# Optimization experiments

Hardware: AMD Instinct MI355X
Metric: run time of the kernel (lower is better)

Reference implementation:

```python
import jax, jax.numpy as jnp
import numpy as np

B, S, D, H = 8, 4096, 1024, 1024


def log_g(x):
    # log of g(x) = where(x>=0, x+0.5, sigmoid(x)); strictly positive
    return jnp.where(x >= 0, jnp.log(jax.nn.relu(x) + 0.5), -jax.nn.softplus(-x))


def mingru_layer(inp, W, b):
    # inp: (B,S,Din), W: (2H,Din), b: (2H,)
    gh = jnp.einsum('bsd,ed->bse', inp, W) + b
    gate, hidden = jnp.split(gh, 2, axis=2)          # each (B,S,H)
    log_z = -jax.nn.softplus(-gate)                   # log sigmoid(gate)
    log_coeffs = -jax.nn.softplus(gate)               # log(1 - sigmoid(gate))
    h0_log = jnp.full((inp.shape[0], 1, gate.shape[2]), jnp.log(0.5), inp.dtype)  # g(0)=0.5
    log_values = jnp.concatenate([h0_log, log_z + log_g(hidden)], axis=1)  # (B,S+1,H)
    # parallel scan in log space
    a_star = jnp.pad(jnp.cumsum(log_coeffs, axis=1), ((0, 0), (1, 0), (0, 0)))  # (B,S+1,H)
    log_h = a_star + jax.lax.cumlogsumexp(log_values - a_star, axis=1)
    return jnp.exp(log_h)[:, 1:]                      # (B,S,H)


def setup_inputs() -> dict:
    key = jax.random.key(0)
    k = jax.random.split(key, 5)
    s = 1.0 / np.sqrt(D)
    return {
        'x': jax.random.normal(k[0], (B, S, D), jnp.float32),
        'W0': jax.random.uniform(k[1], (2 * H, D), jnp.float32, -s, s),
        'b0': jax.random.uniform(k[2], (2 * H,), jnp.float32, -s, s),
        'W1': jax.random.uniform(k[3], (2 * H, H), jnp.float32, -s, s),
        'b1': jax.random.uniform(k[4], (2 * H,), jnp.float32, -s, s),
    }


def reference(x, W0, b0, W1, b1):
    h1 = mingru_layer(x, W0, b0)    # layer 0
    out = mingru_layer(h1, W1, b1)  # layer 1 (last)
    return out                      # (B,S,H)
```

## Files before the change

kernel.cpp:

```cpp
#include <hip/hip_runtime.h>
#include <hip/hip_bf16.h>
#include <stdint.h>


typedef __attribute__((ext_vector_type(8))) short bf16x8;
typedef __attribute__((ext_vector_type(4))) float f32x4;

__device__ __forceinline__ unsigned short f2bf(float f) {
    union { float f; unsigned int u; } x; x.f = f;
    unsigned int r = x.u + 0x7fffu + ((x.u >> 16) & 1u);
    return (unsigned short)(r >> 16);
}
__device__ __forceinline__ float bf2f(unsigned short u) {
    union { unsigned int i; float f; } x; x.i = ((unsigned int)u) << 16;
    return x.f;
}
__device__ __forceinline__ float fsig(float x) {
    return __builtin_amdgcn_rcpf(1.0f + __expf(-x));
}

__device__ __forceinline__ void async_cp16(const void* g, void* lds) {
    __builtin_amdgcn_global_load_lds(
        (const __attribute__((address_space(1))) unsigned int*)g,
        (__attribute__((address_space(3))) unsigned int*)lds, 16, 0, 0);
}

__global__ void f32_to_bf16_k(const float* __restrict__ in,
                              unsigned short* __restrict__ out, int n8) {
    int i = blockIdx.x * blockDim.x + threadIdx.x;
    if (i >= n8) return;
    const float4* p = reinterpret_cast<const float4*>(in);
    float4 a = p[2 * i], b = p[2 * i + 1];
    float f[8] = {a.x, a.y, a.z, a.w, b.x, b.y, b.z, b.w};
    union { unsigned short s[8]; uint4 v; } u;
#pragma unroll
    for (int j = 0; j < 8; ++j) u.s[j] = f2bf(f[j]);
    *reinterpret_cast<uint4*>(out + (size_t)i * 8) = u.v;
}

__global__ __launch_bounds__(512, 2) void gemm256(
    const short* __restrict__ A, const short* __restrict__ Wt,
    const float* __restrict__ bias, unsigned short* __restrict__ C,
    int M, int N, int K)
{
    __shared__ __align__(16) short lds_a[32768];
    __shared__ __align__(16) short lds_b[32768];

    const int tid  = threadIdx.x;
    const int lane = tid & 63;
    const int wave = tid >> 6;
    const int wm   = wave >> 2;
    const int wn   = wave & 3;

    const int bid  = blockIdx.x;
    const int slot = bid >> 3;
    const int mt   = (bid & 7) * 16 + (slot >> 3);
    const int nt   = slot & 7;
    const int m0   = mt * 256, n0 = nt * 256;

    const int g    = lane >> 4;
    const int x7   = lane & 7;
    const int r15  = lane & 15;
    const int aoff0 = (wm*128 + r15)*64 + (( g      ^ x7) * 8);
    const int aoff1 = (wm*128 + r15)*64 + (((4 + g) ^ x7) * 8);
    const int boff0 = (wn*64  + r15)*64 + (( g      ^ x7) * 8);
    const int boff1 = (wn*64  + r15)*64 + (((4 + g) ^ x7) * 8);

    const int srow = wave*16 + (lane >> 3);
    const int lch  = (lane & 7) ^ (lane >> 3);
    const short* pAs = A  + (size_t)(m0 + srow) * K + lch*8;
    const short* pBs = Wt + (size_t)(n0 + srow) * K + lch*8;
    const int dst = wave * 1024;

    f32x4  acc[8][4] = {};
    bf16x8 Ar[4][2];
    bf16x8 Br[2][2][2];

#define STG_A(h, kt) do { \
    async_cp16(pAs + (size_t)((h)*128    )*K + (kt)*64, lds_a + ((((kt)&1)*16384) + (h)*8192 + dst      )); \
    async_cp16(pAs + (size_t)((h)*128 + 8)*K + (kt)*64, lds_a + ((((kt)&1)*16384) + (h)*8192 + dst + 512)); } while (0)
#define STG_B(h, kt) do { \
    async_cp16(pBs + (size_t)((h)*128    )*K + (kt)*64, lds_b + ((((kt)&1)*16384) + (h)*8192 + dst      )); \
    async_cp16(pBs + (size_t)((h)*128 + 8)*K + (kt)*64, lds_b + ((((kt)&1)*16384) + (h)*8192 + dst + 512)); } while (0)

#define READ_A(mh, buf) do { _Pragma("unroll") \
    for (int f = 0; f < 4; ++f) { \
        Ar[f][0] = *reinterpret_cast<const bf16x8*>(lds_a + (buf)*16384 + (mh)*4096 + f*1024 + aoff0); \
        Ar[f][1] = *reinterpret_cast<const bf16x8*>(lds_a + (buf)*16384 + (mh)*4096 + f*1024 + aoff1); } } while (0)
#define READ_B(nh, buf) do { _Pragma("unroll") \
    for (int n = 0; n < 2; ++n) { \
        Br[nh][n][0] = *reinterpret_cast<const bf16x8*>(lds_b + (buf)*16384 + (nh)*2048 + n*1024 + boff0); \
        Br[nh][n][1] = *reinterpret_cast<const bf16x8*>(lds_b + (buf)*16384 + (nh)*2048 + n*1024 + boff1); } } while (0)

#define MFMA_Q(mh, nh) do { \
    __builtin_amdgcn_s_setprio(1); \
    _Pragma("unroll") for (int f = 0; f < 4; ++f) \
    _Pragma("unroll") for (int n = 0; n < 2; ++n) { \
        acc[(mh)*4+f][(nh)*2+n] = __builtin_amdgcn_mfma_f32_16x16x32_bf16(Ar[f][0], Br[nh][n][0], acc[(mh)*4+f][(nh)*2+n], 0, 0, 0); \
        acc[(mh)*4+f][(nh)*2+n] = __builtin_amdgcn_mfma_f32_16x16x32_bf16(Ar[f][1], Br[nh][n][1], acc[(mh)*4+f][(nh)*2+n], 0, 0, 0); } \
    __builtin_amdgcn_s_setprio(0); } while (0)

#define SB() __builtin_amdgcn_sched_barrier(0)
#define BAR1() do { SB(); __builtin_amdgcn_s_barrier(); \
    asm volatile("s_waitcnt lgkmcnt(0)" ::: "memory"); SB(); } while (0)
#define BAR2() do { SB(); __builtin_amdgcn_s_barrier(); \
    asm volatile("" ::: "memory"); SB(); } while (0)
#define VMW(n) asm volatile("s_waitcnt vmcnt(" #n ")" ::: "memory")

    STG_B(0, 0); STG_B(1, 0); STG_A(0, 0); STG_A(1, 0);
    STG_B(0, 1); STG_B(1, 1);
    VMW(4);
    BAR2();

#pragma unroll 1
    for (int i = 0; i < 7; ++i) {
        const int kt = 2 * i;
        READ_A(0,0); READ_B(0,0); STG_A(0, kt+1); BAR1(); MFMA_Q(0,0);         BAR2();
        READ_B(1,0);              STG_A(1, kt+1); BAR1(); MFMA_Q(0,1);         BAR2();
        READ_A(1,0);              STG_B(0, kt+2); BAR1(); MFMA_Q(1,0);         BAR2();
                                  STG_B(1, kt+2); BAR1(); MFMA_Q(1,1); VMW(4); BAR2();
        READ_A(0,1); READ_B(0,1); STG_A(0, kt+2); BAR1(); MFMA_Q(0,0);         BAR2();
        READ_B(1,1);              STG_A(1, kt+2); BAR1(); MFMA_Q(0,1);         BAR2();
        READ_A(1,1);              STG_B(0, kt+3); BAR1(); MFMA_Q(1,0);         BAR2();
                                  STG_B(1, kt+3); BAR1(); MFMA_Q(1,1); VMW(4); BAR2();
    }
    READ_A(0,0); READ_B(0,0); STG_A(0, 15); BAR1(); MFMA_Q(0,0);         BAR2();
    READ_B(1,0);              STG_A(1, 15); BAR1(); MFMA_Q(0,1);         BAR2();
    READ_A(1,0);                            BAR1(); MFMA_Q(1,0);         BAR2();
                                            BAR1(); MFMA_Q(1,1); VMW(0); BAR2();
    READ_A(0,1); READ_B(0,1);               BAR1(); MFMA_Q(0,0);         BAR2();
    READ_B(1,1);                            BAR1(); MFMA_Q(0,1);         BAR2();
    READ_A(1,1);                            BAR1(); MFMA_Q(1,0);         BAR2();
                                            BAR1(); MFMA_Q(1,1);        BAR2();

    const int quad  = lane >> 4;
    const int ccol0 = n0 + wn*64 + r15;
    const size_t crow0 = (size_t)(m0 + wm*128 + quad*4);
    float bv[4];
#pragma unroll
    for (int n = 0; n < 4; ++n) bv[n] = bias[ccol0 + n*16];
#pragma unroll
    for (int f = 0; f < 8; ++f)
#pragma unroll
        for (int r = 0; r < 4; ++r) {
            const size_t row = crow0 + f*16 + r;
#pragma unroll
            for (int n = 0; n < 4; ++n)
                C[row * N + ccol0 + n*16] = f2bf(acc[f][n][r] + bv[n]);
        }
#undef STG_A
#undef STG_B
#undef READ_A
#undef READ_B
#undef MFMA_Q
#undef SB
#undef BAR1
#undef BAR2
#undef VMW
}

__global__ void scan_partial(const unsigned short* __restrict__ gh,
                             float* __restrict__ P, float* __restrict__ V) {
    const int h4 = threadIdx.x;
    const int j = blockIdx.y, b = blockIdx.z;
    const size_t base = ((size_t)b * 4096 + (size_t)j * 32) * 2048 + h4 * 4;
    float p[4] = {1, 1, 1, 1}, hl[4] = {0, 0, 0, 0};
#pragma unroll 8
    for (int t = 0; t < 32; ++t) {
        ushort4 g  = *reinterpret_cast<const ushort4*>(gh + base + (size_t)t * 2048);
        ushort4 hd = *reinterpret_cast<const ushort4*>(gh + base + (size_t)t * 2048 + 1024);
        const unsigned short ga[4] = {g.x, g.y, g.z, g.w};
        const unsigned short ha[4] = {hd.x, hd.y, hd.z, hd.w};
#pragma unroll
        for (int c = 0; c < 4; ++c) {
            float gf = bf2f(ga[c]), hf = bf2f(ha[c]);
            float z  = fsig(gf);
            float cc = 1.0f - z;
            float gv = (hf >= 0.0f) ? (hf + 0.5f) : fsig(hf);
            p[c]  = p[c] * cc;
            hl[c] = cc * hl[c] + z * gv;
        }
    }
    const int ch = b * 1024 + h4 * 4;
    *reinterpret_cast<float4*>(P + (size_t)j * 8192 + ch) = make_float4(p[0], p[1], p[2], p[3]);
    *reinterpret_cast<float4*>(V + (size_t)j * 8192 + ch) = make_float4(hl[0], hl[1], hl[2], hl[3]);
}

__global__ void scan_combine(const float* __restrict__ P,
                             const float* __restrict__ V,
                             float* __restrict__ hstart) {
    const int c4 = blockIdx.x * blockDim.x + threadIdx.x;
    float4 h = make_float4(0.5f, 0.5f, 0.5f, 0.5f);
#pragma unroll 8
    for (int j = 0; j < 128; ++j) {
        *reinterpret_cast<float4*>(hstart + (size_t)j * 8192 + c4 * 4) = h;
        float4 pp = *reinterpret_cast<const float4*>(P + (size_t)j * 8192 + c4 * 4);
        float4 vv = *reinterpret_cast<const float4*>(V + (size_t)j * 8192 + c4 * 4);
        h.x = pp.x * h.x + vv.x; h.y = pp.y * h.y + vv.y;
        h.z = pp.z * h.z + vv.z; h.w = pp.w * h.w + vv.w;
    }
}

template <bool BF16OUT, typename OUT>
__global__ void scan_final(const unsigned short* __restrict__ gh,
                           const float* __restrict__ hstart,
                           OUT* __restrict__ out) {
    const int h4 = threadIdx.x;
    const int j = blockIdx.y, b = blockIdx.z;
    const size_t base  = ((size_t)b * 4096 + (size_t)j * 32) * 2048 + h4 * 4;
    const size_t obase = ((size_t)b * 4096 + (size_t)j * 32) * 1024 + h4 * 4;
    float4 hq = *reinterpret_cast<const float4*>(hstart + (size_t)j * 8192 + b * 1024 + h4 * 4);
    float hv[4] = {hq.x, hq.y, hq.z, hq.w};
#pragma unroll 8
    for (int t = 0; t < 32; ++t) {
        ushort4 g  = *reinterpret_cast<const ushort4*>(gh + base + (size_t)t * 2048);
        ushort4 hd = *reinterpret_cast<const ushort4*>(gh + base + (size_t)t * 2048 + 1024);
        const unsigned short ga[4] = {g.x, g.y, g.z, g.w};
        const unsigned short ha[4] = {hd.x, hd.y, hd.z, hd.w};
#pragma unroll
        for (int c = 0; c < 4; ++c) {
            float gf = bf2f(ga[c]), hf = bf2f(ha[c]);
            float z  = fsig(gf);
            float cc = 1.0f - z;
            float gv = (hf >= 0.0f) ? (hf + 0.5f) : fsig(hf);
            hv[c] = cc * hv[c] + z * gv;
        }
        if (BF16OUT) {
            ushort4 o = make_ushort4(f2bf(hv[0]), f2bf(hv[1]), f2bf(hv[2]), f2bf(hv[3]));
            *reinterpret_cast<ushort4*>((unsigned short*)out + obase + (size_t)t * 1024) = o;
        } else {
            *reinterpret_cast<float4*>((float*)out + obase + (size_t)t * 1024) =
                make_float4(hv[0], hv[1], hv[2], hv[3]);
        }
    }
}

extern "C" void kernel_launch(void* const* d_in, const int* in_sizes, int n_in,
                              void* d_out, int out_size, void* d_ws, size_t ws_size,
                              hipStream_t stream) {
    const float* x  = (const float*)d_in[0];
    const float* W0 = (const float*)d_in[1];
    const float* b0 = (const float*)d_in[2];
    const float* W1 = (const float*)d_in[3];
    const float* b1 = (const float*)d_in[4];
    float* out = (float*)d_out;

    char* ws = (char*)d_ws;
    unsigned short* gh   = (unsigned short*)ws;
    unsigned short* abuf = (unsigned short*)(ws + 0x08000000);
    unsigned short* w0b  = (unsigned short*)(ws + 0x0C000000);
    unsigned short* w1b  = (unsigned short*)(ws + 0x0C400000);
    float*          P    = (float*)(ws + 0x0C800000);
    float*          V    = (float*)(ws + 0x0CC00000);
    float*          hst  = (float*)(ws + 0x0D000000);

    const int M = 32768, N = 2048, K = 1024;

    f32_to_bf16_k<<<4194304 / 256, 256, 0, stream>>>(x,  abuf, 4194304);
    f32_to_bf16_k<<<262144 / 256, 256, 0, stream>>>(W0, w0b, 262144);
    f32_to_bf16_k<<<262144 / 256, 256, 0, stream>>>(W1, w1b, 262144);

    dim3 sg(1, 128, 8);

    gemm256<<<1024, 512, 0, stream>>>((const short*)abuf, (const short*)w0b, b0, gh, M, N, K);
    scan_partial<<<sg, 256, 0, stream>>>(gh, P, V);
    scan_combine<<<8, 256, 0, stream>>>(P, V, hst);
    scan_final<true, unsigned short><<<sg, 256, 0, stream>>>(gh, hst, abuf);

    gemm256<<<1024, 512, 0, stream>>>((const short*)abuf, (const short*)w1b, b1, gh, M, N, K);
    scan_partial<<<sg, 256, 0, stream>>>(gh, P, V);
    scan_combine<<<8, 256, 0, stream>>>(P, V, hst);
    scan_final<false, float><<<sg, 256, 0, stream>>>(gh, hst, out);
}
```

Measured before the change: 666.9 us.

## Restructure GEMM main loop barriers and widen scan combine parallelism

The GEMM inner loop is rebuilt from eight double-barrier phases per k-step pair into single-barrier phases. Global-to-LDS staging of A is moved to a per-block end point with a vmcnt wait, and the staging order and prologue depth change. The goal is to cut barrier count and give loads more room to overlap with MFMA work, at the risk of LDS hazards if buffer reuse timing is now wrong. Separately, scan_combine is split from float4-per-thread over 8 blocks into scalar-per-thread over 32 blocks, trading vector loads for more parallelism in its serial chain.

```diff
diff --git a/kernel.cpp b/kernel.cpp
--- a/kernel.cpp
+++ b/kernel.cpp
@@ -101,37 +101,50 @@
     __builtin_amdgcn_s_setprio(0); } while (0)
 
 #define SB() __builtin_amdgcn_sched_barrier(0)
-#define BAR1() do { SB(); __builtin_amdgcn_s_barrier(); \
-    asm volatile("s_waitcnt lgkmcnt(0)" ::: "memory"); SB(); } while (0)
-#define BAR2() do { SB(); __builtin_amdgcn_s_barrier(); \
-    asm volatile("" ::: "memory"); SB(); } while (0)
-#define VMW(n) asm volatile("s_waitcnt vmcnt(" #n ")" ::: "memory")
-
-    STG_B(0, 0); STG_B(1, 0); STG_A(0, 0); STG_A(1, 0);
-    STG_B(0, 1); STG_B(1, 1);
-    VMW(4);
-    BAR2();
+#define NOP ((void)0)
+#define PH0(b, STG) do { STG; READ_A(0,b); READ_B(0,b); SB(); \
+    __builtin_amdgcn_s_barrier(); \
+    asm volatile("s_waitcnt lgkmcnt(0)" ::: "memory"); SB(); MFMA_Q(0,0); } while (0)
+#define PH1(b) do { READ_B(1,b); SB(); \
+    __builtin_amdgcn_s_barrier(); \
+    asm volatile("s_waitcnt lgkmcnt(0)" ::: "memory"); SB(); MFMA_Q(0,1); } while (0)
+#define PH2(b) do { READ_A(1,b); SB(); \
+    __builtin_amdgcn_s_barrier(); \
+    asm volatile("s_waitcnt lgkmcnt(0)" ::: "memory"); SB(); MFMA_Q(1,0); } while (0)
+#define PH3(b, STG) do { STG; SB(); \
+    __builtin_amdgcn_s_barrier(); \
+    asm volatile("s_waitcnt lgkmcnt(0)" ::: "memory"); SB(); MFMA_Q(1,1); } while (0)
+#define ENDBLK(n, S1, S2) do { S1; S2; SB(); \
+    asm volatile("s_waitcnt vmcnt(" #n ")" ::: "memory"); \
+    __builtin_amdgcn_s_barrier(); SB(); } while (0)
+
+    STG_A(0, 0); STG_A(1, 0); STG_B(0, 0); STG_B(1, 0);
+    STG_B(0, 1); STG_A(0, 1); STG_A(1, 1);
+    ENDBLK(6, NOP, NOP);
 
 #pragma unroll 1
     for (int i = 0; i < 7; ++i) {
         const int kt = 2 * i;
-        READ_A(0,0); READ_B(0,0); STG_A(0, kt+1); BAR1(); MFMA_Q(0,0);         BAR2();
-        READ_B(1,0);              STG_A(1, kt+1); BAR1(); MFMA_Q(0,1);         BAR2();
-        READ_A(1,0);              STG_B(0, kt+2); BAR1(); MFMA_Q(1,0);         BAR2();
-                                  STG_B(1, kt+2); BAR1(); MFMA_Q(1,1); VMW(4); BAR2();
-        READ_A(0,1); READ_B(0,1); STG_A(0, kt+2); BAR1(); MFMA_Q(0,0);         BAR2();
-        READ_B(1,1);              STG_A(1, kt+2); BAR1(); MFMA_Q(0,1);         BAR2();
-        READ_A(1,1);              STG_B(0, kt+3); BAR1(); MFMA_Q(1,0);         BAR2();
-                                  STG_B(1, kt+3); BAR1(); MFMA_Q(1,1); VMW(4); BAR2();
-    }
-    READ_A(0,0); READ_B(0,0); STG_A(0, 15); BAR1(); MFMA_Q(0,0);         BAR2();
-    READ_B(1,0);              STG_A(1, 15); BAR1(); MFMA_Q(0,1);         BAR2();
-    READ_A(1,0);                            BAR1(); MFMA_Q(1,0);         BAR2();
-                                            BAR1(); MFMA_Q(1,1); VMW(0); BAR2();
-    READ_A(0,1); READ_B(0,1);               BAR1(); MFMA_Q(0,0);         BAR2();
-    READ_B(1,1);                            BAR1(); MFMA_Q(0,1);         BAR2();
-    READ_A(1,1);                            BAR1(); MFMA_Q(1,0);         BAR2();
-                                            BAR1(); MFMA_Q(1,1);        BAR2();
+        PH0(0, STG_B(1, kt + 1));
+        PH1(0);
+        PH2(0);
+        PH3(0, STG_B(0, kt + 2));
+        ENDBLK(6, STG_A(0, kt + 2), STG_A(1, kt + 2));
+        PH0(1, STG_B(1, kt + 2));
+        PH1(1);
+        PH2(1);
+        PH3(1, STG_B(0, kt + 3));
+        ENDBLK(6, STG_A(0, kt + 3), STG_A(1, kt + 3));
+    }
+    PH0(0, STG_B(1, 15));
+    PH1(0);
+    PH2(0);
+    PH3(0, NOP);
+    ENDBLK(0, NOP, NOP);
+    PH0(1, NOP);
+    PH1(1);
+    PH2(1);
+    PH3(1, NOP);
 
     const int quad  = lane >> 4;
     const int ccol0 = n0 + wn*64 + r15;
@@ -154,9 +167,12 @@
 #undef READ_B
 #undef MFMA_Q
 #undef SB
-#undef BAR1
-#undef BAR2
-#undef VMW
+#undef NOP
+#undef PH0
+#undef PH1
+#undef PH2
+#undef PH3
+#undef ENDBLK
 }
 
 __global__ void scan_partial(const unsigned short* __restrict__ gh,
@@ -189,15 +205,12 @@
 __global__ void scan_combine(const float* __restrict__ P,
                              const float* __restrict__ V,
                              float* __restrict__ hstart) {
-    const int c4 = blockIdx.x * blockDim.x + threadIdx.x;
-    float4 h = make_float4(0.5f, 0.5f, 0.5f, 0.5f);
+    const int ch = blockIdx.x * blockDim.x + threadIdx.x;
+    float h = 0.5f;
 #pragma unroll 8
     for (int j = 0; j < 128; ++j) {
-        *reinterpret_cast<float4*>(hstart + (size_t)j * 8192 + c4 * 4) = h;
-        float4 pp = *reinterpret_cast<const float4*>(P + (size_t)j * 8192 + c4 * 4);
-        float4 vv = *reinterpret_cast<const float4*>(V + (size_t)j * 8192 + c4 * 4);
-        h.x = pp.x * h.x + vv.x; h.y = pp.y * h.y + vv.y;
-        h.z = pp.z * h.z + vv.z; h.w = pp.w * h.w + vv.w;
+        hstart[(size_t)j * 8192 + ch] = h;
+        h = P[(size_t)j * 8192 + ch] * h + V[(size_t)j * 8192 + ch];
     }
 }
 
@@ -264,11 +277,11 @@
 
     gemm256<<<1024, 512, 0, stream>>>((const short*)abuf, (const short*)w0b, b0, gh, M, N, K);
     scan_partial<<<sg, 256, 0, stream>>>(gh, P, V);
-    scan_combine<<<8, 256, 0, stream>>>(P, V, hst);
+    scan_combine<<<32, 256, 0, stream>>>(P, V, hst);
     scan_final<true, unsigned short><<<sg, 256, 0, stream>>>(gh, hst, abuf);
 
     gemm256<<<1024, 512, 0, stream>>>((const short*)abuf, (const short*)w1b, b1, gh, M, N, K);
     scan_partial<<<sg, 256, 0, stream>>>(gh, P, V);
-    scan_combine<<<8, 256, 0, stream>>>(P, V, hst);
+    scan_combine<<<32, 256, 0, stream>>>(P, V, hst);
     scan_final<false, float><<<sg, 256, 0, stream>>>(gh, hst, out);
 }
```

New measurement: 650.5 us. 1.03x faster.
